# Kernel tuning notes

Hardware: AMD Instinct MI355X
Metric: run time of the kernel (lower is better)

Reference implementation:

```python
import jax, jax.numpy as jnp
import numpy as np

N = 8192


def setup_inputs() -> dict:
    key = jax.random.key(0)
    k1, k2 = jax.random.split(key)
    # dense symmetric-style weight matrix (adjacency/Laplacian analog)
    info_mtx = jax.random.uniform(k1, (N, N), dtype=jnp.float32)
    state = jax.random.normal(k2, (N,), dtype=jnp.float32)
    return {"info_mtx": info_mtx, "state": state}


def reference(info_mtx, state):
    # pb_type == 'maxcut': G = -0.5 * info_mtx
    G = -0.5 * info_mtx
    # Original python loop: sum over i<=j of G[i,j]*s_i*s_j (diag term linear in s_i)
    offdiag = jnp.triu(G, k=1)                     # strictly upper triangle [N,N]
    diag = jnp.diagonal(G)                         # [N]
    quad = jnp.dot(state, offdiag @ state)         # sum_{i<j} G_ij s_i s_j
    lin = jnp.dot(diag, state)                     # sum_i G_ii s_i
    total = -(quad + lin)
    num_edges = jnp.sum(info_mtx) / 2.0
    return num_edges / 2.0 - total
```

## Files before the change

kernel.cpp:

```cpp
#include <hip/hip_runtime.h>


static constexpr int N_DIM  = 8192;
static constexpr int VPR    = N_DIM / 4;
static constexpr int BLOCK  = 256;
static constexpr int ITERS  = VPR / BLOCK;
static constexpr int GRID   = 1024;
static constexpr int RPB    = N_DIM / GRID;
static constexpr int FBLOCK = 1024;

__global__ __launch_bounds__(BLOCK) void ising_rows_kernel(
    const float4* __restrict__ mtx4,
    const float*  __restrict__ state,
    float*        __restrict__ partial)
{
    const int tid = threadIdx.x;
    const float4* __restrict__ s4 = (const float4*)state;

    float4 s[ITERS];
#pragma unroll
    for (int k = 0; k < ITERS; ++k)
        s[k] = s4[tid + (k << 8)];

    const int row0 = blockIdx.x * RPB;
    const float4* __restrict__ base = mtx4 + (size_t)row0 * VPR;

    float acc = 0.0f;

#pragma unroll 1
    for (int g = 0; g < RPB; ++g) {
        const int   row = row0 + g;
        const int   d   = row >> 2;
        const float p   = -0.5f * state[row];

        float4 m[ITERS];
#pragma unroll
        for (int k = 0; k < ITERS; ++k)
            m[k] = base[(size_t)g * VPR + tid + (k << 8)];

        float accA = 0.0f, q0 = 0.0f, q1 = 0.0f;
#pragma unroll
        for (int k = 0; k < ITERS; ++k) {
            const int    v  = tid + (k << 8);
            const float4 mm = m[k];
            const float4 sj = s[k];
            accA += (mm.x + mm.y) + (mm.z + mm.w);
            if (v > d) {
                q0 = fmaf(mm.x, sj.x, q0);
                q1 = fmaf(mm.y, sj.y, q1);
                q0 = fmaf(mm.z, sj.z, q0);
                q1 = fmaf(mm.w, sj.w, q1);
            } else if (v == d) {
                const int j0 = v << 2;
                float w;
                w = (j0 + 0 > row) ? sj.x : ((j0 + 0 == row) ? 1.0f : 0.0f);
                q0 = fmaf(mm.x, w, q0);
                w = (j0 + 1 > row) ? sj.y : ((j0 + 1 == row) ? 1.0f : 0.0f);
                q1 = fmaf(mm.y, w, q1);
                w = (j0 + 2 > row) ? sj.z : ((j0 + 2 == row) ? 1.0f : 0.0f);
                q0 = fmaf(mm.z, w, q0);
                w = (j0 + 3 > row) ? sj.w : ((j0 + 3 == row) ? 1.0f : 0.0f);
                q1 = fmaf(mm.w, w, q1);
            }
        }
        acc = fmaf(0.25f, accA, fmaf(p, q0 + q1, acc));
    }

    for (int off = 32; off > 0; off >>= 1)
        acc += __shfl_down(acc, off, 64);

    __shared__ float lds[BLOCK / 64];
    const int lane = tid & 63;
    const int wave = tid >> 6;
    if (lane == 0) lds[wave] = acc;
    __syncthreads();
    if (tid == 0)
        partial[blockIdx.x] = (lds[0] + lds[1]) + (lds[2] + lds[3]);
}

__global__ __launch_bounds__(FBLOCK) void ising_final_kernel(
    const float* __restrict__ partial,
    float*       __restrict__ out)
{
    float acc = partial[threadIdx.x];

    for (int off = 32; off > 0; off >>= 1)
        acc += __shfl_down(acc, off, 64);

    __shared__ float lds[FBLOCK / 64];
    const int lane = threadIdx.x & 63;
    const int wave = threadIdx.x >> 6;
    if (lane == 0) lds[wave] = acc;
    __syncthreads();
    if (threadIdx.x == 0) {
        float sum = 0.0f;
#pragma unroll
        for (int w = 0; w < FBLOCK / 64; ++w) sum += lds[w];
        out[0] = sum;
    }
}

extern "C" void kernel_launch(void* const* d_in, const int* in_sizes, int n_in,
                              void* d_out, int out_size, void* d_ws, size_t ws_size,
                              hipStream_t stream) {
    const float* mtx   = (const float*)d_in[0];
    const float* state = (const float*)d_in[1];
    float* out     = (float*)d_out;
    float* partial = (float*)d_ws;

    ising_rows_kernel<<<GRID, BLOCK, 0, stream>>>((const float4*)mtx, state, partial);
    ising_final_kernel<<<1, FBLOCK, 0, stream>>>(partial, out);
}
```

Baseline: 357.1 us.

## Restructure row sweep so each block strides rows over one column slice

Each block now owns a 1024-column slice (256 threads × float4) and walks 32 rows spaced 256 apart, instead of processing 8 consecutive full rows. Each thread keeps a single state float4 in registers rather than eight, and the grid doubles to 2048 blocks. The final reduction sums two partials per thread to match. The goal is lower register pressure and higher occupancy, with more loads in flight to better saturate HBM bandwidth. In exchange, row-strided access gives each block scattered 4 KB segments, which may hurt DRAM locality.

```diff
diff --git a/kernel.cpp b/kernel.cpp
--- a/kernel.cpp
+++ b/kernel.cpp
@@ -4,67 +4,52 @@
 static constexpr int N_DIM  = 8192;
 static constexpr int VPR    = N_DIM / 4;
 static constexpr int BLOCK  = 256;
-static constexpr int ITERS  = VPR / BLOCK;
-static constexpr int GRID   = 1024;
-static constexpr int RPB    = N_DIM / GRID;
+static constexpr int GRID   = 2048;
+static constexpr int ITERS  = N_DIM / 256;
 static constexpr int FBLOCK = 1024;
 
-__global__ __launch_bounds__(BLOCK) void ising_rows_kernel(
+__global__ __launch_bounds__(BLOCK) void ising_sweep_kernel(
     const float4* __restrict__ mtx4,
     const float*  __restrict__ state,
     float*        __restrict__ partial)
 {
-    const int tid = threadIdx.x;
-    const float4* __restrict__ s4 = (const float4*)state;
+    const int tid  = threadIdx.x;
+    const int row0 = blockIdx.x >> 3;
+    const int v    = ((blockIdx.x & 7) << 8) + tid;
+    const float4 sj = ((const float4*)state)[v];
+    const float4* __restrict__ colp = mtx4 + v;
 
-    float4 s[ITERS];
-#pragma unroll
-    for (int k = 0; k < ITERS; ++k)
-        s[k] = s4[tid + (k << 8)];
-
-    const int row0 = blockIdx.x * RPB;
-    const float4* __restrict__ base = mtx4 + (size_t)row0 * VPR;
-
-    float acc = 0.0f;
-
-#pragma unroll 1
-    for (int g = 0; g < RPB; ++g) {
-        const int   row = row0 + g;
+    float acc0 = 0.0f, acc1 = 0.0f;
+#pragma unroll 8
+    for (int it = 0; it < ITERS; ++it) {
+        const int   row = row0 + (it << 8);
         const int   d   = row >> 2;
         const float p   = -0.5f * state[row];
+        const float4 mm = colp[(size_t)row * VPR];
 
-        float4 m[ITERS];
-#pragma unroll
-        for (int k = 0; k < ITERS; ++k)
-            m[k] = base[(size_t)g * VPR + tid + (k << 8)];
+        const float accA = (mm.x + mm.y) + (mm.z + mm.w);
 
-        float accA = 0.0f, q0 = 0.0f, q1 = 0.0f;
-#pragma unroll
-        for (int k = 0; k < ITERS; ++k) {
-            const int    v  = tid + (k << 8);
-            const float4 mm = m[k];
-            const float4 sj = s[k];
-            accA += (mm.x + mm.y) + (mm.z + mm.w);
-            if (v > d) {
-                q0 = fmaf(mm.x, sj.x, q0);
-                q1 = fmaf(mm.y, sj.y, q1);
-                q0 = fmaf(mm.z, sj.z, q0);
-                q1 = fmaf(mm.w, sj.w, q1);
-            } else if (v == d) {
-                const int j0 = v << 2;
-                float w;
-                w = (j0 + 0 > row) ? sj.x : ((j0 + 0 == row) ? 1.0f : 0.0f);
-                q0 = fmaf(mm.x, w, q0);
-                w = (j0 + 1 > row) ? sj.y : ((j0 + 1 == row) ? 1.0f : 0.0f);
-                q1 = fmaf(mm.y, w, q1);
-                w = (j0 + 2 > row) ? sj.z : ((j0 + 2 == row) ? 1.0f : 0.0f);
-                q0 = fmaf(mm.z, w, q0);
-                w = (j0 + 3 > row) ? sj.w : ((j0 + 3 == row) ? 1.0f : 0.0f);
-                q1 = fmaf(mm.w, w, q1);
-            }
+        const bool gt = (v > d);
+        float wx = gt ? sj.x : 0.0f;
+        float wy = gt ? sj.y : 0.0f;
+        float wz = gt ? sj.z : 0.0f;
+        float ww = gt ? sj.w : 0.0f;
+        if (v == d) {
+            const int j0 = v << 2;
+            wx = (j0 + 0 > row) ? sj.x : ((j0 + 0 == row) ? 1.0f : 0.0f);
+            wy = (j0 + 1 > row) ? sj.y : ((j0 + 1 == row) ? 1.0f : 0.0f);
+            wz = (j0 + 2 > row) ? sj.z : ((j0 + 2 == row) ? 1.0f : 0.0f);
+            ww = (j0 + 3 > row) ? sj.w : ((j0 + 3 == row) ? 1.0f : 0.0f);
         }
-        acc = fmaf(0.25f, accA, fmaf(p, q0 + q1, acc));
+        float q = mm.x * wx;
+        q = fmaf(mm.y, wy, q);
+        q = fmaf(mm.z, wz, q);
+        q = fmaf(mm.w, ww, q);
+
+        if (it & 1) acc1 = fmaf(0.25f, accA, fmaf(p, q, acc1));
+        else        acc0 = fmaf(0.25f, accA, fmaf(p, q, acc0));
     }
+    float acc = acc0 + acc1;
 
     for (int off = 32; off > 0; off >>= 1)
         acc += __shfl_down(acc, off, 64);
@@ -82,7 +67,7 @@
     const float* __restrict__ partial,
     float*       __restrict__ out)
 {
-    float acc = partial[threadIdx.x];
+    float acc = partial[threadIdx.x] + partial[threadIdx.x + FBLOCK];
 
     for (int off = 32; off > 0; off >>= 1)
         acc += __shfl_down(acc, off, 64);
@@ -108,6 +93,6 @@
     float* out     = (float*)d_out;
     float* partial = (float*)d_ws;
 
-    ising_rows_kernel<<<GRID, BLOCK, 0, stream>>>((const float4*)mtx, state, partial);
+    ising_sweep_kernel<<<GRID, BLOCK, 0, stream>>>((const float4*)mtx, state, partial);
     ising_final_kernel<<<1, FBLOCK, 0, stream>>>(partial, out);
 }
```

After: 365.8 us. 1.02x slower.

## Process two rows per block with nontemporal loads across 4096 blocks

Applied to the files above, without the earlier changes.

Each block now handles a pair of adjacent rows instead of eight rows in a serial loop, which raises the grid to 4096 blocks. Both rows' loads are issued up front as nontemporal loads so more bytes are in flight per thread. The state vector is re-read from cache per element instead of being held in registers. The final reduction is extended to sum four partials per thread, adding block-launch overhead and more partial-sum traffic in exchange for better memory-level parallelism on a bandwidth-bound stream.

```diff
diff --git a/kernel.cpp b/kernel.cpp
--- a/kernel.cpp
+++ b/kernel.cpp
@@ -5,66 +5,80 @@
 static constexpr int VPR    = N_DIM / 4;
 static constexpr int BLOCK  = 256;
 static constexpr int ITERS  = VPR / BLOCK;
-static constexpr int GRID   = 1024;
-static constexpr int RPB    = N_DIM / GRID;
+static constexpr int GRID   = N_DIM / 2;
 static constexpr int FBLOCK = 1024;
 
-__global__ __launch_bounds__(BLOCK) void ising_rows_kernel(
+__device__ __forceinline__ float4 ntload4(const float4* p) {
+    typedef float f32x4 __attribute__((ext_vector_type(4)));
+    const f32x4 v = __builtin_nontemporal_load((const f32x4*)p);
+    return make_float4(v.x, v.y, v.z, v.w);
+}
+
+__global__ __launch_bounds__(BLOCK) void ising_rowpair_kernel(
     const float4* __restrict__ mtx4,
     const float*  __restrict__ state,
     float*        __restrict__ partial)
 {
-    const int tid = threadIdx.x;
-    const float4* __restrict__ s4 = (const float4*)state;
+    const int tid  = threadIdx.x;
+    const int row0 = blockIdx.x << 1;
+    const int row1 = row0 | 1;
+    const int d    = row0 >> 2;
+    const float p0 = -0.5f * state[row0];
+    const float p1 = -0.5f * state[row1];
+    const float4* __restrict__ rp0 = mtx4 + (size_t)row0 * VPR;
+    const float4* __restrict__ rp1 = mtx4 + (size_t)row1 * VPR;
+    const float4* __restrict__ s4  = (const float4*)state;
 
-    float4 s[ITERS];
+    float4 m0[ITERS], m1[ITERS];
 #pragma unroll
     for (int k = 0; k < ITERS; ++k)
-        s[k] = s4[tid + (k << 8)];
+        m0[k] = ntload4(rp0 + tid + (k << 8));
+#pragma unroll
+    for (int k = 0; k < ITERS; ++k)
+        m1[k] = ntload4(rp1 + tid + (k << 8));
 
-    const int row0 = blockIdx.x * RPB;
-    const float4* __restrict__ base = mtx4 + (size_t)row0 * VPR;
+    float accA0 = 0.0f, accA1 = 0.0f;
+    float q0 = 0.0f, q1 = 0.0f;
+#pragma unroll
+    for (int k = 0; k < ITERS; ++k) {
+        const int    v  = tid + (k << 8);
+        const float4 a  = m0[k];
+        const float4 b  = m1[k];
+        const float4 sj = s4[v];
+        accA0 += (a.x + a.y) + (a.z + a.w);
+        accA1 += (b.x + b.y) + (b.z + b.w);
+        if (v > d) {
+            q0 = fmaf(a.x, sj.x, q0);
+            q0 = fmaf(a.y, sj.y, q0);
+            q0 = fmaf(a.z, sj.z, q0);
+            q0 = fmaf(a.w, sj.w, q0);
+            q1 = fmaf(b.x, sj.x, q1);
+            q1 = fmaf(b.y, sj.y, q1);
+            q1 = fmaf(b.z, sj.z, q1);
+            q1 = fmaf(b.w, sj.w, q1);
+        } else if (v == d) {
+            const int j0 = v << 2;
+            float w;
+            w = (j0 + 0 > row0) ? sj.x : ((j0 + 0 == row0) ? 1.0f : 0.0f);
+            q0 = fmaf(a.x, w, q0);
+            w = (j0 + 1 > row0) ? sj.y : ((j0 + 1 == row0) ? 1.0f : 0.0f);
+            q0 = fmaf(a.y, w, q0);
+            w = (j0 + 2 > row0) ? sj.z : ((j0 + 2 == row0) ? 1.0f : 0.0f);
+            q0 = fmaf(a.z, w, q0);
+            w = (j0 + 3 > row0) ? sj.w : ((j0 + 3 == row0) ? 1.0f : 0.0f);
+            q0 = fmaf(a.w, w, q0);
+            w = (j0 + 0 > row1) ? sj.x : ((j0 + 0 == row1) ? 1.0f : 0.0f);
+            q1 = fmaf(b.x, w, q1);
+            w = (j0 + 1 > row1) ? sj.y : ((j0 + 1 == row1) ? 1.0f : 0.0f);
+            q1 = fmaf(b.y, w, q1);
+            w = (j0 + 2 > row1) ? sj.z : ((j0 + 2 == row1) ? 1.0f : 0.0f);
+            q1 = fmaf(b.z, w, q1);
+            w = (j0 + 3 > row1) ? sj.w : ((j0 + 3 == row1) ? 1.0f : 0.0f);
+            q1 = fmaf(b.w, w, q1);
+        }
+    }
 
-    float acc = 0.0f;
-
-#pragma unroll 1
-    for (int g = 0; g < RPB; ++g) {
-        const int   row = row0 + g;
-        const int   d   = row >> 2;
-        const float p   = -0.5f * state[row];
-
-        float4 m[ITERS];
-#pragma unroll
-        for (int k = 0; k < ITERS; ++k)
-            m[k] = base[(size_t)g * VPR + tid + (k << 8)];
-
-        float accA = 0.0f, q0 = 0.0f, q1 = 0.0f;
-#pragma unroll
-        for (int k = 0; k < ITERS; ++k) {
-            const int    v  = tid + (k << 8);
-            const float4 mm = m[k];
-            const float4 sj = s[k];
-            accA += (mm.x + mm.y) + (mm.z + mm.w);
-            if (v > d) {
-                q0 = fmaf(mm.x, sj.x, q0);
-                q1 = fmaf(mm.y, sj.y, q1);
-                q0 = fmaf(mm.z, sj.z, q0);
-                q1 = fmaf(mm.w, sj.w, q1);
-            } else if (v == d) {
-                const int j0 = v << 2;
-                float w;
-                w = (j0 + 0 > row) ? sj.x : ((j0 + 0 == row) ? 1.0f : 0.0f);
-                q0 = fmaf(mm.x, w, q0);
-                w = (j0 + 1 > row) ? sj.y : ((j0 + 1 == row) ? 1.0f : 0.0f);
-                q1 = fmaf(mm.y, w, q1);
-                w = (j0 + 2 > row) ? sj.z : ((j0 + 2 == row) ? 1.0f : 0.0f);
-                q0 = fmaf(mm.z, w, q0);
-                w = (j0 + 3 > row) ? sj.w : ((j0 + 3 == row) ? 1.0f : 0.0f);
-                q1 = fmaf(mm.w, w, q1);
-            }
-        }
-        acc = fmaf(0.25f, accA, fmaf(p, q0 + q1, acc));
-    }
+    float acc = fmaf(0.25f, accA0 + accA1, fmaf(p0, q0, p1 * q1));
 
     for (int off = 32; off > 0; off >>= 1)
         acc += __shfl_down(acc, off, 64);
@@ -82,7 +96,10 @@
     const float* __restrict__ partial,
     float*       __restrict__ out)
 {
-    float acc = partial[threadIdx.x];
+    float acc = 0.0f;
+#pragma unroll
+    for (int k = 0; k < GRID / FBLOCK; ++k)
+        acc += partial[threadIdx.x + k * FBLOCK];
 
     for (int off = 32; off > 0; off >>= 1)
         acc += __shfl_down(acc, off, 64);
@@ -108,6 +125,6 @@
     float* out     = (float*)d_out;
     float* partial = (float*)d_ws;
 
-    ising_rows_kernel<<<GRID, BLOCK, 0, stream>>>((const float4*)mtx, state, partial);
+    ising_rowpair_kernel<<<GRID, BLOCK, 0, stream>>>((const float4*)mtx, state, partial);
     ising_final_kernel<<<1, FBLOCK, 0, stream>>>(partial, out);
 }
```

After: 332.4 us. 6.9% less time.

## Double-buffer matrix rows in LDS via async global-to-LDS loads

Applied to the files above, without the earlier changes.

Row loads now go straight from global memory into a two-slot LDS buffer using global_load_lds, replacing loads into registers. The next row is prefetched while the current row is being reduced, with a block barrier each row. The grid is halved to 512 blocks of 16 rows, and the final reduction is resized to match. The goal is to overlap memory latency with compute. The cost is 64KB of LDS per block, which limits occupancy, plus a barrier every row.

```diff
diff --git a/kernel.cpp b/kernel.cpp
--- a/kernel.cpp
+++ b/kernel.cpp
@@ -4,45 +4,62 @@
 static constexpr int N_DIM  = 8192;
 static constexpr int VPR    = N_DIM / 4;
 static constexpr int BLOCK  = 256;
-static constexpr int ITERS  = VPR / BLOCK;
-static constexpr int GRID   = 1024;
+static constexpr int GRID   = 512;
 static constexpr int RPB    = N_DIM / GRID;
-static constexpr int FBLOCK = 1024;
+static constexpr int FBLOCK = 512;
 
-__global__ __launch_bounds__(BLOCK) void ising_rows_kernel(
+__device__ __forceinline__ void dma16(const void* g, void* l) {
+    __builtin_amdgcn_global_load_lds(
+        (const __attribute__((address_space(1))) void*)g,
+        (__attribute__((address_space(3)))       void*)l,
+        16, 0, 2 );
+}
+
+__global__ __launch_bounds__(BLOCK) void ising_dma_kernel(
     const float4* __restrict__ mtx4,
     const float*  __restrict__ state,
     float*        __restrict__ partial)
 {
+    __shared__ float4 buf[2][VPR];
     const int tid = threadIdx.x;
+    const int w   = tid >> 6;
+
     const float4* __restrict__ s4 = (const float4*)state;
-
-    float4 s[ITERS];
+    float4 s[8];
 #pragma unroll
-    for (int k = 0; k < ITERS; ++k)
+    for (int k = 0; k < 8; ++k)
         s[k] = s4[tid + (k << 8)];
 
     const int row0 = blockIdx.x * RPB;
     const float4* __restrict__ base = mtx4 + (size_t)row0 * VPR;
 
+#pragma unroll
+    for (int k = 0; k < 8; ++k)
+        dma16(base + (k << 8) + tid, &buf[0][(k << 8) + (w << 6)]);
+
     float acc = 0.0f;
 
 #pragma unroll 1
     for (int g = 0; g < RPB; ++g) {
+        const int cur = g & 1;
+        __syncthreads();
+
+        if (g + 1 < RPB) {
+            const float4* nb = base + (size_t)(g + 1) * VPR;
+#pragma unroll
+            for (int k = 0; k < 8; ++k)
+                dma16(nb + (k << 8) + tid, &buf[cur ^ 1][(k << 8) + (w << 6)]);
+        }
+
         const int   row = row0 + g;
         const int   d   = row >> 2;
         const float p   = -0.5f * state[row];
 
-        float4 m[ITERS];
-#pragma unroll
-        for (int k = 0; k < ITERS; ++k)
-            m[k] = base[(size_t)g * VPR + tid + (k << 8)];
-
         float accA = 0.0f, q0 = 0.0f, q1 = 0.0f;
 #pragma unroll
-        for (int k = 0; k < ITERS; ++k) {
+        for (int k = 0; k < 8; ++k) {
             const int    v  = tid + (k << 8);
-            const float4 mm = m[k];
+            const float4 mm = buf[cur][v];
             const float4 sj = s[k];
             accA += (mm.x + mm.y) + (mm.z + mm.w);
             if (v > d) {
@@ -52,15 +69,15 @@
                 q1 = fmaf(mm.w, sj.w, q1);
             } else if (v == d) {
                 const int j0 = v << 2;
-                float w;
-                w = (j0 + 0 > row) ? sj.x : ((j0 + 0 == row) ? 1.0f : 0.0f);
-                q0 = fmaf(mm.x, w, q0);
-                w = (j0 + 1 > row) ? sj.y : ((j0 + 1 == row) ? 1.0f : 0.0f);
-                q1 = fmaf(mm.y, w, q1);
-                w = (j0 + 2 > row) ? sj.z : ((j0 + 2 == row) ? 1.0f : 0.0f);
-                q0 = fmaf(mm.z, w, q0);
-                w = (j0 + 3 > row) ? sj.w : ((j0 + 3 == row) ? 1.0f : 0.0f);
-                q1 = fmaf(mm.w, w, q1);
+                float ww;
+                ww = (j0 + 0 > row) ? sj.x : ((j0 + 0 == row) ? 1.0f : 0.0f);
+                q0 = fmaf(mm.x, ww, q0);
+                ww = (j0 + 1 > row) ? sj.y : ((j0 + 1 == row) ? 1.0f : 0.0f);
+                q1 = fmaf(mm.y, ww, q1);
+                ww = (j0 + 2 > row) ? sj.z : ((j0 + 2 == row) ? 1.0f : 0.0f);
+                q0 = fmaf(mm.z, ww, q0);
+                ww = (j0 + 3 > row) ? sj.w : ((j0 + 3 == row) ? 1.0f : 0.0f);
+                q1 = fmaf(mm.w, ww, q1);
             }
         }
         acc = fmaf(0.25f, accA, fmaf(p, q0 + q1, acc));
@@ -71,8 +88,7 @@
 
     __shared__ float lds[BLOCK / 64];
     const int lane = tid & 63;
-    const int wave = tid >> 6;
-    if (lane == 0) lds[wave] = acc;
+    if (lane == 0) lds[w] = acc;
     __syncthreads();
     if (tid == 0)
         partial[blockIdx.x] = (lds[0] + lds[1]) + (lds[2] + lds[3]);
@@ -95,7 +111,7 @@
     if (threadIdx.x == 0) {
         float sum = 0.0f;
 #pragma unroll
-        for (int w = 0; w < FBLOCK / 64; ++w) sum += lds[w];
+        for (int wv = 0; wv < FBLOCK / 64; ++wv) sum += lds[wv];
         out[0] = sum;
     }
 }
@@ -108,6 +124,6 @@
     float* out     = (float*)d_out;
     float* partial = (float*)d_ws;
 
-    ising_rows_kernel<<<GRID, BLOCK, 0, stream>>>((const float4*)mtx, state, partial);
+    ising_dma_kernel<<<GRID, BLOCK, 0, stream>>>((const float4*)mtx, state, partial);
     ising_final_kernel<<<1, FBLOCK, 0, stream>>>(partial, out);
 }
```

Measured after the change: 331.5 us. -7.1%, faster.
